# Kernel optimization log

Hardware: AMD Instinct MI355X
Metric: run time of the kernel (lower is better)

## Reference

```python
import jax, jax.numpy as jnp
import numpy as np

# ---- constants from module defaults ----
IMG, PS, STRIDE, C_IN = 224, 16, 8, 1
NP1D = (IMG - PS) // STRIDE + 1          # 27
NUM_PATCHES = NP1D * NP1D                # 729
EMBED = 64
N_INPUT = NUM_PATCHES * EMBED            # 46656
N_HIDDEN = 1000                          # d_model
N_RNN = 100
N_STEPS = 5
BETA, THR = 0.8, 0.5
BETA_R, THR_R = 0.95, 1.0
LM_SPN = 0.0058
ALPHA = 2.0  # snntorch ATan surrogate default

@jax.custom_vjp
def spike(x):
    return (x > 0).astype(x.dtype)

def _spike_fwd(x):
    return spike(x), x

def _spike_bwd(x, g):
    # snntorch ATan surrogate gradient
    return (g * (ALPHA / 2.0) / (1.0 + (jnp.pi / 2.0 * ALPHA * x) ** 2),)

spike.defvjp(_spike_fwd, _spike_bwd)

def extract_patches(x):
    # x: [B, C, H, W] -> [B, num_patches, C*PS*PS] matching torch unfold+permute+flatten
    B, C, H, W = x.shape
    idx = (jnp.arange(NP1D)[:, None] * STRIDE + jnp.arange(PS)).reshape(-1)  # [NP1D*PS]
    t = x[:, :, idx, :].reshape(B, C, NP1D, PS, W)
    t = t[..., idx].reshape(B, C, NP1D, PS, NP1D, PS)
    t = t.transpose(0, 2, 4, 1, 3, 5)  # [B, nh, nw, C, ph, pw]
    return t.reshape(B, NUM_PATCHES, C * PS * PS)

def setup_inputs() -> dict:
    key = jax.random.key(0)
    ks = jax.random.split(key, 12)
    def lin(k, fi, fo):
        kw, kb = jax.random.split(k)
        s = 1.0 / np.sqrt(fi)
        return (jax.random.uniform(kw, (fi, fo), jnp.float32, -s, s),
                jax.random.uniform(kb, (fo,), jnp.float32, -s, s))
    W_pe, b_pe = lin(ks[0], C_IN * PS * PS, EMBED)
    pos_embed = 0.02 * jax.random.normal(ks[1], (1, NUM_PATCHES, EMBED), jnp.float32)
    W1, b1 = lin(ks[2], N_INPUT, N_HIDDEN)
    W2, b2 = lin(ks[3], N_HIDDEN, N_HIDDEN)
    W3, b3 = lin(ks[4], N_HIDDEN, N_HIDDEN)
    WR, bR = lin(ks[5], N_HIDDEN, N_RNN)
    Vw, Vb = lin(ks[6], N_RNN, N_RNN)      # RLeaky recurrent linear
    Wq, bq = lin(ks[7], N_RNN, N_HIDDEN)
    Wk, bk = lin(ks[8], N_HIDDEN, N_HIDDEN)
    Wv, bv = lin(ks[9], N_HIDDEN, N_HIDDEN)
    Wo, bo = lin(ks[10], N_HIDDEN, 1)       # cross_last=True -> output_proj to 1
    data = jax.random.normal(ks[11], (32, C_IN, IMG, IMG), jnp.float32)
    return {"data": data, "W_pe": W_pe, "b_pe": b_pe, "pos_embed": pos_embed,
            "W1": W1, "b1": b1, "W2": W2, "b2": b2, "W3": W3, "b3": b3,
            "WR": WR, "bR": bR, "Vw": Vw, "Vb": Vb,
            "Wq": Wq, "bq": bq, "Wk": Wk, "bk": bk, "Wv": Wv, "bv": bv,
            "Wo": Wo, "bo": bo}

def _forward(data, W_pe, b_pe, pos_embed, W1, b1, W2, b2, W3, b3,
             WR, bR, Vw, Vb, Wq, bq, Wk, bk, Wv, bv, Wo, bo):
    B = data.shape[0]
    patches = extract_patches(data)                      # [B, 729, 256]
    x = patches @ W_pe + b_pe + pos_embed               # [B, 729, 64]
    x_flat = x.reshape(B, -1)                            # [B, 46656]
    cur1 = x_flat @ W1 + b1                              # constant across steps
    scale = jnp.sqrt(jnp.asarray(N_HIDDEN, jnp.float32))  # head_dim = d_model (1 head)

    def leaky(mem, cur, beta=BETA, thr=THR):
        reset = jax.lax.stop_gradient(spike(mem - thr))
        mem = beta * mem + cur - reset * thr
        return mem, spike(mem - thr)

    def step(carry, t):
        mem1, mem2, mem3, spk_r, mem_r, mem_out, total, prev, reg = carry
        # layers[:2] call -- first Leaky1 update
        mem1, spk1 = leaky(mem1, cur1)
        # layers[:7] call -- Leaky1 state updated a SECOND time (same x_flat)
        mem1, spk1b = leaky(mem1, cur1)
        mem2, spk2 = leaky(mem2, spk1b @ W2 + b2)
        mem3, spk3 = leaky(mem3, spk2 @ W3 + b3)  # Dropout is identity in eval
        total = total + spk1.mean() + spk3.mean()
        # RLeaky (beta=0.95, threshold=1.0, subtract reset, recurrent linear)
        rlin = spk1 @ WR + bR
        reset_r = jax.lax.stop_gradient(spike(mem_r - THR_R))
        mem_r = BETA_R * mem_r + rlin + spk_r @ Vw + Vb - reset_r * THR_R
        spk_r = spike(mem_r - THR_R)
        total = total + spk_r.mean()
        # cross-attention: feature dim acts as the sequence dim (seq=1 in view)
        q = spk_r @ Wq + bq                               # [B, 1000]
        k = spk3 @ Wk + bk                                # [B, 1000]
        v = spk3 @ Wv + bv                                # [B, 1000]
        probs = jax.nn.softmax(q[:, :, None] * k[:, None, :] / scale, axis=-1)  # [B,1000,1000]
        att = jnp.einsum('bij,bj->bi', probs, v) @ Wo + bo  # [B, 1]
        mem_out, spk_out = leaky(mem_out, att)
        mem_out = jax.lax.stop_gradient(mem_out)          # .detach() in source
        total = total + spk_out.mean()
        reg = reg + LM_SPN * total + jnp.where(t > 0, LM_SPN * jnp.abs(total - prev), 0.0)
        return (mem1, mem2, mem3, spk_r, mem_r, mem_out, total, total, reg), spk_out

    z = jnp.float32(0.0)
    init = (jnp.zeros((B, N_HIDDEN)), jnp.zeros((B, N_HIDDEN)), jnp.zeros((B, N_HIDDEN)),
            jnp.zeros((B, N_RNN)), jnp.zeros((B, N_RNN)), jnp.zeros((B, 1)), z, z, z)
    carry, spk_rec = jax.lax.scan(step, init, jnp.arange(N_STEPS))
    out = spk_rec.sum(0)[:, 0] / N_STEPS                  # [B]
    reg_norm = carry[-1] / N_STEPS
    return out, reg_norm

def reference(data, W_pe, b_pe, pos_embed, W1, b1, W2, b2, W3, b3,
              WR, bR, Vw, Vb, Wq, bq, Wk, bk, Wv, bv, Wo, bo):
    return _forward(data, W_pe, b_pe, pos_embed, W1, b1, W2, b2, W3, b3,
                    WR, bR, Vw, Vb, Wq, bq, Wk, bk, Wv, bv, Wo, bo)
```

## Files before the change

kernel.cpp:

```cpp
#include <hip/hip_runtime.h>

#define OFF_X     0
#define OFF_CUR1  1492992
#define OFF_MEM1  1524992
#define OFF_MEM2  1556992
#define OFF_MEM3  1588992
#define OFF_SPK1B 1652992
#define OFF_MEMR  1844992
#define OFF_SPKR  1848192
#define OFF_MEMO  1851392
#define OFF_PATT  1851424
#define OFF_CNT   1851680
#define OFF_OACC  1851700
#define OFF_SC    1851732
#define OFF_TICK  1851736
#define OFF_PART  1851744
#define OFF_PG2   OFF_PART
#define OFF_PG3   (OFF_PART + 800000)
#define OFF_PKK   (OFF_PART + 1600000)
#define OFF_PVV   (OFF_PART + 2400000)
#define OFF_M2B   (OFF_PART + 3200000)
#define OFF_M3B   (OFF_PART + 3232000)

static constexpr float kBETA  = 0.8f;
static constexpr float kTHR   = 0.5f;
static constexpr float kBETAR = 0.95f;
static constexpr float kTHRR  = 1.0f;
static constexpr float kLM    = 0.0058f;

__global__ void k_init(float* ws) {
    int idx = blockIdx.x * 256 + threadIdx.x;
    if (idx < 96000) {
        ws[OFF_MEM1 + idx] = 0.f;
    } else {
        int j = idx - 96000;
        if (j < 6752) ws[OFF_MEMR + j] = 0.f;
    }
}

__global__ __launch_bounds__(64) void k_patch(
    const float* __restrict__ data, const float* __restrict__ Wpe,
    const float* __restrict__ bpe, const float* __restrict__ pos,
    float* __restrict__ xf)
{
    int b = blockIdx.x, pr = blockIdx.y;
    int tid = threadIdx.x;
    const float* db = data + (size_t)b * 50176 + pr * 1792;
    float bb = bpe[tid];
    float acc[27];
    #pragma unroll
    for (int pc = 0; pc < 27; ++pc)
        acc[pc] = bb + pos[(pr * 27 + pc) * 64 + tid];
    #pragma unroll 2
    for (int c = 0; c < 256; ++c) {
        float w = Wpe[c * 64 + tid];
        const float* row = db + (c >> 4) * 224 + (c & 15);
        #pragma unroll
        for (int pc = 0; pc < 27; ++pc)
            acc[pc] = fmaf(row[pc * 8], w, acc[pc]);
    }
    size_t obase = (size_t)b * 46656 + (size_t)pr * 27 * 64 + tid;
    #pragma unroll
    for (int pc = 0; pc < 27; ++pc)
        xf[obase + (size_t)pc * 64] = acc[pc];
}

__global__ __launch_bounds__(256) void k_gemm1_part(
    const float* __restrict__ xf, const float* __restrict__ W1,
    float* __restrict__ part, int tpc)
{
    int chunk = blockIdx.x;
    int hg = blockIdx.y;
    int t0 = chunk * tpc;
    int t1 = t0 + tpc; if (t1 > 729) t1 = 729;
    int tid = threadIdx.x;
    __shared__ float xs[2048];
    float acc[32][2];
    #pragma unroll
    for (int b = 0; b < 32; ++b) { acc[b][0] = 0.f; acc[b][1] = 0.f; }

    const int hbase = hg * 500;
    const bool ok1 = (tid + 256) < 500;
    const int h0 = hbase + tid;
    const int h1 = hbase + (ok1 ? tid + 256 : 0);
    for (int tt = t0; tt < t1; ++tt) {
        int i0 = tt * 64;
        __syncthreads();
        for (int l = tid; l < 2048; l += 256)
            xs[l] = xf[(size_t)(l >> 6) * 46656 + i0 + (l & 63)];
        __syncthreads();
        for (int ii4 = 0; ii4 < 16; ++ii4) {
            int i = i0 + ii4 * 4;
            const float* c0 = W1 + (size_t)i * 1000 + h0;
            const float* c1 = W1 + (size_t)i * 1000 + h1;
            float w0a = c0[0], w1a = c0[1000], w2a = c0[2000], w3a = c0[3000];
            float w0b = ok1 ? c1[0]    : 0.f;
            float w1b = ok1 ? c1[1000] : 0.f;
            float w2b = ok1 ? c1[2000] : 0.f;
            float w3b = ok1 ? c1[3000] : 0.f;
            #pragma unroll
            for (int b = 0; b < 32; ++b) {
                float4 xv = *reinterpret_cast<const float4*>(&xs[b * 64 + ii4 * 4]);
                float a0 = acc[b][0], a1 = acc[b][1];
                a0 = fmaf(xv.x, w0a, a0);  a1 = fmaf(xv.x, w0b, a1);
                a0 = fmaf(xv.y, w1a, a0);  a1 = fmaf(xv.y, w1b, a1);
                a0 = fmaf(xv.z, w2a, a0);  a1 = fmaf(xv.z, w2b, a1);
                a0 = fmaf(xv.w, w3a, a0);  a1 = fmaf(xv.w, w3b, a1);
                acc[b][0] = a0; acc[b][1] = a1;
            }
        }
    }
    float* pc = part + (size_t)chunk * 32000 + hbase;
    #pragma unroll
    for (int b = 0; b < 32; ++b) {
        pc[b * 1000 + tid] = acc[b][0];
        if (ok1) pc[b * 1000 + tid + 256] = acc[b][1];
    }
}

__global__ void k_gemm1_reduce(const float* __restrict__ part,
                               const float* __restrict__ b1,
                               float* __restrict__ cur1, int nchunk)
{
    int idx = blockIdx.x * 128 + threadIdx.x;
    if (idx >= 32000) return;
    int h = idx % 1000;
    float a0 = b1[h], a1 = 0.f, a2 = 0.f, a3 = 0.f;
    int c = 0;
    for (; c + 4 <= nchunk; c += 4) {
        a0 += part[(size_t)c * 32000 + idx];
        a1 += part[(size_t)(c + 1) * 32000 + idx];
        a2 += part[(size_t)(c + 2) * 32000 + idx];
        a3 += part[(size_t)(c + 3) * 32000 + idx];
    }
    for (; c < nchunk; ++c) a0 += part[(size_t)c * 32000 + idx];
    cur1[idx] = (a0 + a1) + (a2 + a3);
}

__global__ __launch_bounds__(512) void k_stepR(
    const float* __restrict__ cur1, float* __restrict__ mem1,
    float* __restrict__ spk1b,
    const float* __restrict__ WR, const float* __restrict__ bR,
    const float* __restrict__ Vw, const float* __restrict__ Vb,
    float* __restrict__ mem_r, float* __restrict__ spk_r,
    float* cnt0, float* cnt2)
{
    int b = blockIdx.x;
    int tid = threadIdx.x;
    __shared__ float s1[1000];
    __shared__ float sr[100];
    __shared__ float red2[4][128];
    __shared__ float csum[8];

    float localc = 0.f;
    if (tid < 250) {
        int base = b * 1000 + tid * 4;
        float4 m4 = *reinterpret_cast<const float4*>(&mem1[base]);
        float4 c4 = *reinterpret_cast<const float4*>(&cur1[base]);
        float mm[4] = {m4.x, m4.y, m4.z, m4.w};
        float cc[4] = {c4.x, c4.y, c4.z, c4.w};
        float mb[4], sb[4];
        #pragma unroll
        for (int q = 0; q < 4; ++q) {
            float m = mm[q], c = cc[q];
            float r1 = (m - kTHR > 0.f) ? kTHR : 0.f;
            float ma = __fsub_rn(__fadd_rn(__fmul_rn(kBETA, m), c), r1);
            float s  = (ma - kTHR > 0.f) ? 1.f : 0.f;
            float r2 = __fmul_rn(s, kTHR);
            float mv = __fsub_rn(__fadd_rn(__fmul_rn(kBETA, ma), c), r2);
            sb[q] = (mv - kTHR > 0.f) ? 1.f : 0.f;
            mb[q] = mv;
            s1[tid * 4 + q] = s;
            localc += s;
        }
        *reinterpret_cast<float4*>(&mem1[base])  = make_float4(mb[0], mb[1], mb[2], mb[3]);
        *reinterpret_cast<float4*>(&spk1b[base]) = make_float4(sb[0], sb[1], sb[2], sb[3]);
    }
    if (tid < 100) sr[tid] = spk_r[b * 100 + tid];
    for (int off = 32; off; off >>= 1) localc += __shfl_down(localc, off, 64);
    if ((tid & 63) == 0) csum[tid >> 6] = localc;
    __syncthreads();
    if (tid == 0) {
        float cs = 0.f;
        #pragma unroll
        for (int w = 0; w < 8; ++w) cs += csum[w];
        atomicAdd(cnt0, cs);
    }

    int ks = tid >> 7, hh = tid & 127;
    float p = 0.f;
    if (hh < 100) {
        const float* wp = WR + (size_t)(ks * 250) * 100 + hh;
        int j0 = ks * 250;
        #pragma unroll 5
        for (int j = 0; j < 250; ++j) p = fmaf(s1[j0 + j], wp[(size_t)j * 100], p);
    }
    red2[ks][hh] = p;
    __syncthreads();
    float s = 0.f;
    if (tid < 100) {
        float acc = bR[tid] + ((red2[0][tid] + red2[1][tid]) + (red2[2][tid] + red2[3][tid]));
        float rec = 0.f;
        for (int j = 0; j < 100; ++j) rec = fmaf(sr[j], Vw[j * 100 + tid], rec);
        float m = mem_r[b * 100 + tid];
        float r = (m - kTHRR > 0.f) ? kTHRR : 0.f;
        float mn = __fsub_rn(__fadd_rn(__fadd_rn(__fadd_rn(__fmul_rn(kBETAR, m), acc), rec), Vb[tid]), r);
        s = (mn - kTHRR > 0.f) ? 1.f : 0.f;
        mem_r[b * 100 + tid] = mn;
        spk_r[b * 100 + tid] = s;
    }
    unsigned long long msk = __ballot(s > 0.5f);
    if ((tid & 63) == 0) {
        int pc2 = __popcll(msk);
        if (pc2) atomicAdd(cnt2, (float)pc2);
    }
}

__global__ __launch_bounds__(256) void k_gsp(
    const float* __restrict__ A, const float* __restrict__ W,
    float* __restrict__ part)
{
    int hb = blockIdx.x, kc = blockIdx.y, bg = blockIdx.z;
    int tid = threadIdx.x;
    int j0 = kc * 40;
    __shared__ __align__(16) float al[320];
    __shared__ float redg[8 * 128];
    for (int l = tid; l < 320; l += 256)
        al[l] = A[(size_t)(bg * 8 + (l & 7)) * 1000 + j0 + (l >> 3)];
    __syncthreads();
    int ks = tid >> 7, hh = tid & 127;
    float acc[8];
    #pragma unroll
    for (int b = 0; b < 8; ++b) acc[b] = 0.f;
    if (hh < 125) {
        int h = hb * 125 + hh;
        const float* Wp = W + (size_t)(j0 + ks * 20) * 1000 + h;
        const float4* abase = reinterpret_cast<const float4*>(&al[ks * 20 * 8]);
        #pragma unroll 4
        for (int jj = 0; jj < 20; ++jj) {
            float w = Wp[(size_t)jj * 1000];
            const float4* a4 = abase + jj * 2;
            #pragma unroll
            for (int q = 0; q < 2; ++q) {
                float4 av = a4[q];
                acc[q * 4 + 0] = fmaf(av.x, w, acc[q * 4 + 0]);
                acc[q * 4 + 1] = fmaf(av.y, w, acc[q * 4 + 1]);
                acc[q * 4 + 2] = fmaf(av.z, w, acc[q * 4 + 2]);
                acc[q * 4 + 3] = fmaf(av.w, w, acc[q * 4 + 3]);
            }
        }
    }
    if (ks == 1 && hh < 125) {
        #pragma unroll
        for (int b = 0; b < 8; ++b) redg[b * 128 + hh] = acc[b];
    }
    __syncthreads();
    if (ks == 0 && hh < 125) {
        int h = hb * 125 + hh;
        float* pp = part + (size_t)kc * 32000 + (size_t)(bg * 8) * 1000 + h;
        #pragma unroll
        for (int b = 0; b < 8; ++b) pp[(size_t)b * 1000] = acc[b] + redg[b * 128 + hh];
    }
}

template <bool COUNT>
__global__ __launch_bounds__(256) void k_gspred(
    const float* __restrict__ pin, const float* __restrict__ bias,
    const float* __restrict__ mem_old, float* __restrict__ mem_new,
    const float* __restrict__ W, float* __restrict__ pout, float* cnt)
{
    int hs = blockIdx.x, kc = blockIdx.y, bg = blockIdx.z;
    int tid = threadIdx.x;
    int j0 = kc * 40;
    __shared__ __align__(16) float al[320];
    __shared__ float redg[8 * 128];
    __shared__ float csum[4];
    float localc = 0.f;
    for (int e = tid; e < 320; e += 256) {
        int jj = e % 40, bi = e / 40;
        int idx = (bg * 8 + bi) * 1000 + j0 + jj;
        float a = bias[j0 + jj];
        #pragma unroll 5
        for (int c = 0; c < 25; ++c) a += pin[(size_t)c * 32000 + idx];
        float m = mem_old[idx];
        float r = (m - kTHR > 0.f) ? kTHR : 0.f;
        float mn = __fsub_rn(__fadd_rn(__fmul_rn(kBETA, m), a), r);
        float s = (mn - kTHR > 0.f) ? 1.f : 0.f;
        al[jj * 8 + bi] = s;
        if (hs == 0) { mem_new[idx] = mn; localc += s; }
    }
    if (COUNT) {
        for (int off = 32; off; off >>= 1) localc += __shfl_down(localc, off, 64);
        if ((tid & 63) == 0) csum[tid >> 6] = localc;
    }
    __syncthreads();
    if (COUNT && tid == 0 && hs == 0) {
        float tot = csum[0] + csum[1] + csum[2] + csum[3];
        if (tot != 0.f) atomicAdd(cnt, tot);
    }
    int ks = tid >> 7, hh = tid & 127;
    float acc[8];
    #pragma unroll
    for (int b = 0; b < 8; ++b) acc[b] = 0.f;
    if (hh < 125) {
        int h = hs * 125 + hh;
        const float* Wp = W + (size_t)(j0 + ks * 20) * 1000 + h;
        const float4* abase = reinterpret_cast<const float4*>(&al[ks * 20 * 8]);
        #pragma unroll 4
        for (int jj = 0; jj < 20; ++jj) {
            float w = Wp[(size_t)jj * 1000];
            const float4* a4 = abase + jj * 2;
            #pragma unroll
            for (int q = 0; q < 2; ++q) {
                float4 av = a4[q];
                acc[q * 4 + 0] = fmaf(av.x, w, acc[q * 4 + 0]);
                acc[q * 4 + 1] = fmaf(av.y, w, acc[q * 4 + 1]);
                acc[q * 4 + 2] = fmaf(av.z, w, acc[q * 4 + 2]);
                acc[q * 4 + 3] = fmaf(av.w, w, acc[q * 4 + 3]);
            }
        }
    }
    if (ks == 1 && hh < 125) {
        #pragma unroll
        for (int b = 0; b < 8; ++b) redg[b * 128 + hh] = acc[b];
    }
    __syncthreads();
    if (ks == 0 && hh < 125) {
        int h = hs * 125 + hh;
        float* pp = pout + (size_t)kc * 32000 + (size_t)(bg * 8) * 1000 + h;
        #pragma unroll
        for (int b = 0; b < 8; ++b) pp[(size_t)b * 1000] = acc[b] + redg[b * 128 + hh];
    }
}

__global__ __launch_bounds__(256) void k_gspred_kv(
    const float* __restrict__ pin, const float* __restrict__ bias,
    const float* __restrict__ mem_old, float* __restrict__ mem_new,
    const float* __restrict__ Wk, const float* __restrict__ Wv,
    float* __restrict__ pk, float* __restrict__ pv, float* cnt)
{
    int hs = blockIdx.x, kc = blockIdx.y, bg = blockIdx.z;
    int tid = threadIdx.x;
    int j0 = kc * 40;
    __shared__ __align__(16) float al[320];
    __shared__ float redk[8 * 128];
    __shared__ float redv[8 * 128];
    __shared__ float csum[4];
    float localc = 0.f;
    for (int e = tid; e < 320; e += 256) {
        int jj = e % 40, bi = e / 40;
        int idx = (bg * 8 + bi) * 1000 + j0 + jj;
        float a = bias[j0 + jj];
        #pragma unroll 5
        for (int c = 0; c < 25; ++c) a += pin[(size_t)c * 32000 + idx];
        float m = mem_old[idx];
        float r = (m - kTHR > 0.f) ? kTHR : 0.f;
        float mn = __fsub_rn(__fadd_rn(__fmul_rn(kBETA, m), a), r);
        float s = (mn - kTHR > 0.f) ? 1.f : 0.f;
        al[jj * 8 + bi] = s;
        if (hs == 0) { mem_new[idx] = mn; localc += s; }
    }
    for (int off = 32; off; off >>= 1) localc += __shfl_down(localc, off, 64);
    if ((tid & 63) == 0) csum[tid >> 6] = localc;
    __syncthreads();
    if (tid == 0 && hs == 0) {
        float tot = csum[0] + csum[1] + csum[2] + csum[3];
        if (tot != 0.f) atomicAdd(cnt, tot);
    }
    int ks = tid >> 7, hh = tid & 127;
    float ak[8], av2[8];
    #pragma unroll
    for (int b = 0; b < 8; ++b) { ak[b] = 0.f; av2[b] = 0.f; }
    if (hh < 125) {
        int h = hs * 125 + hh;
        const float* wkp = Wk + (size_t)(j0 + ks * 20) * 1000 + h;
        const float* wvp = Wv + (size_t)(j0 + ks * 20) * 1000 + h;
        const float4* abase = reinterpret_cast<const float4*>(&al[ks * 20 * 8]);
        #pragma unroll 4
        for (int jj = 0; jj < 20; ++jj) {
            float wk = wkp[(size_t)jj * 1000];
            float wv = wvp[(size_t)jj * 1000];
            const float4* a4 = abase + jj * 2;
            #pragma unroll
            for (int q = 0; q < 2; ++q) {
                float4 av = a4[q];
                ak[q * 4 + 0] = fmaf(av.x, wk, ak[q * 4 + 0]);
                ak[q * 4 + 1] = fmaf(av.y, wk, ak[q * 4 + 1]);
                ak[q * 4 + 2] = fmaf(av.z, wk, ak[q * 4 + 2]);
                ak[q * 4 + 3] = fmaf(av.w, wk, ak[q * 4 + 3]);
                av2[q * 4 + 0] = fmaf(av.x, wv, av2[q * 4 + 0]);
                av2[q * 4 + 1] = fmaf(av.y, wv, av2[q * 4 + 1]);
                av2[q * 4 + 2] = fmaf(av.z, wv, av2[q * 4 + 2]);
                av2[q * 4 + 3] = fmaf(av.w, wv, av2[q * 4 + 3]);
            }
        }
    }
    if (ks == 1 && hh < 125) {
        #pragma unroll
        for (int b = 0; b < 8; ++b) { redk[b * 128 + hh] = ak[b]; redv[b * 128 + hh] = av2[b]; }
    }
    __syncthreads();
    if (ks == 0 && hh < 125) {
        int h = hs * 125 + hh;
        float* ppk = pk + (size_t)kc * 32000 + (size_t)(bg * 8) * 1000 + h;
        float* ppv = pv + (size_t)kc * 32000 + (size_t)(bg * 8) * 1000 + h;
        #pragma unroll
        for (int b = 0; b < 8; ++b) {
            ppk[(size_t)b * 1000] = ak[b] + redk[b * 128 + hh];
            ppv[(size_t)b * 1000] = av2[b] + redv[b * 128 + hh];
        }
    }
}

__global__ __launch_bounds__(512) void k_attnred(
    const float* __restrict__ pkk, const float* __restrict__ pvv,
    const float* __restrict__ bk, const float* __restrict__ bv,
    const float* __restrict__ spkr, const float* __restrict__ Wq,
    const float* __restrict__ bq, const float* __restrict__ Wo,
    const float* __restrict__ bo,
    float* __restrict__ patt, float* __restrict__ memo,
    float* __restrict__ oacc, const float* __restrict__ cnt,
    float* __restrict__ sc, float* __restrict__ dout,
    unsigned int* __restrict__ tick, int t)
{
    int it = blockIdx.x, b = blockIdx.y;
    int tid = threadIdx.x;
    __shared__ float kk[1000], vv[1000];
    __shared__ float sr[100];
    __shared__ float red[512];
    __shared__ float pden[512], pnum[512];
    __shared__ int isLast;
    float pmax = -3.4e38f, pmin = 3.4e38f;
    if (tid < 100) sr[tid] = spkr[b * 100 + tid];
    for (int h = tid; h < 1000; h += 512) {
        int idx = b * 1000 + h;
        float ak = bk[h], av = bv[h];
        #pragma unroll 5
        for (int c = 0; c < 25; ++c) {
            ak += pkk[(size_t)c * 32000 + idx];
            av += pvv[(size_t)c * 32000 + idx];
        }
        kk[h] = ak; vv[h] = av;
        pmax = fmaxf(pmax, ak);
        pmin = fminf(pmin, ak);
    }
    red[tid] = pmax;
    __syncthreads();
    for (int s2 = 256; s2 > 0; s2 >>= 1) {
        if (tid < s2) red[tid] = fmaxf(red[tid], red[tid + s2]);
        __syncthreads();
    }
    float kmax = red[0];
    __syncthreads();
    red[tid] = pmin;
    __syncthreads();
    for (int s2 = 256; s2 > 0; s2 >>= 1) {
        if (tid < s2) red[tid] = fminf(red[tid], red[tid + s2]);
        __syncthreads();
    }
    float kmin = red[0];
    __syncthreads();

    int quarter = tid >> 7, lane = tid & 127;
    float den = 0.f, num = 0.f;
    if (lane < 125) {
        int i = it * 125 + lane;
        float qi = bq[i];
        for (int j = 0; j < 100; ++j) qi = fmaf(sr[j], Wq[j * 1000 + i], qi);
        float qs = qi / 31.62277660168379f;
        float m = (qs >= 0.f) ? qs * kmax : qs * kmin;
        int jb = quarter * 250;
        for (int j = 0; j < 250; ++j) {
            float e = __expf(fmaf(qs, kk[jb + j], -m));
            den += e;
            num = fmaf(e, vv[jb + j], num);
        }
    }
    pden[tid] = den; pnum[tid] = num;
    __syncthreads();
    float pw = 0.f;
    if (tid < 125) {
        float dsum = (pden[tid] + pden[tid + 128]) + (pden[tid + 256] + pden[tid + 384]);
        float nsum = (pnum[tid] + pnum[tid + 128]) + (pnum[tid + 256] + pnum[tid + 384]);
        pw = (nsum / dsum) * Wo[it * 125 + tid];
    }
    red[tid] = (tid < 125) ? pw : 0.f;
    __syncthreads();
    for (int s2 = 256; s2 > 0; s2 >>= 1) {
        if (tid < s2) red[tid] += red[tid + s2];
        __syncthreads();
    }
    if (tid == 0) patt[b * 8 + it] = red[0];
    __syncthreads();
    if (tid == 0) {
        __threadfence();
        unsigned r = atomicAdd(tick, 1u);
        isLast = (r == 255u) ? 1 : 0;
    }
    __syncthreads();
    if (isLast && tid < 64) {
        __threadfence();
        float s = 0.f;
        if (tid < 32) {
            float a = bo[0];
            for (int itx = 0; itx < 8; ++itx) a += patt[tid * 8 + itx];
            float m = memo[tid];
            float r = (m - kTHR > 0.f) ? kTHR : 0.f;
            float mn = __fsub_rn(__fadd_rn(__fmul_rn(kBETA, m), a), r);
            memo[tid] = mn;
            s = (mn - kTHR > 0.f) ? 1.f : 0.f;
            float oa = oacc[tid] + s;
            oacc[tid] = oa;
            if (t == 4) dout[tid] = oa / 5.0f;
        }
        unsigned long long msk = __ballot(s > 0.5f);
        float co = (float)__popcll(msk);
        if (tid == 0) {
            float total = sc[0];
            float prev = total;
            total = __fadd_rn(total, __fdiv_rn(cnt[0], 32000.f));
            total = __fadd_rn(total, __fdiv_rn(cnt[1], 32000.f));
            total = __fadd_rn(total, __fdiv_rn(cnt[2], 3200.f));
            total = __fadd_rn(total, __fdiv_rn(co, 32.f));
            float reg = sc[1];
            reg = __fadd_rn(reg, __fmul_rn(kLM, total));
            if (t > 0) reg = __fadd_rn(reg, __fmul_rn(kLM, fabsf(__fsub_rn(total, prev))));
            sc[0] = total; sc[1] = reg;
            if (t == 4) dout[32] = reg / 5.0f;
        }
    }
}

extern "C" void kernel_launch(void* const* d_in, const int* in_sizes, int n_in,
                              void* d_out, int out_size, void* d_ws, size_t ws_size,
                              hipStream_t stream)
{
    const float* data = (const float*)d_in[0];
    const float* Wpe  = (const float*)d_in[1];
    const float* bpe  = (const float*)d_in[2];
    const float* pos  = (const float*)d_in[3];
    const float* W1   = (const float*)d_in[4];
    const float* b1   = (const float*)d_in[5];
    const float* W2   = (const float*)d_in[6];
    const float* b2   = (const float*)d_in[7];
    const float* W3   = (const float*)d_in[8];
    const float* b3   = (const float*)d_in[9];
    const float* WR   = (const float*)d_in[10];
    const float* bR   = (const float*)d_in[11];
    const float* Vw   = (const float*)d_in[12];
    const float* Vb   = (const float*)d_in[13];
    const float* Wq   = (const float*)d_in[14];
    const float* bq   = (const float*)d_in[15];
    const float* Wk   = (const float*)d_in[16];
    const float* bk   = (const float*)d_in[17];
    const float* Wv   = (const float*)d_in[18];
    const float* bv   = (const float*)d_in[19];
    const float* Wo   = (const float*)d_in[20];
    const float* bo   = (const float*)d_in[21];

    float* ws = (float*)d_ws;
    float* dout = (float*)d_out;

    float* xf    = ws + OFF_X;
    float* cur1  = ws + OFF_CUR1;
    float* mem1  = ws + OFF_MEM1;
    float* mem2a = ws + OFF_MEM2;
    float* mem3a = ws + OFF_MEM3;
    float* spk1b = ws + OFF_SPK1B;
    float* memr  = ws + OFF_MEMR;
    float* spkr  = ws + OFF_SPKR;
    float* memo  = ws + OFF_MEMO;
    float* patt  = ws + OFF_PATT;
    float* cntb  = ws + OFF_CNT;
    float* oacc  = ws + OFF_OACC;
    float* sc    = ws + OFF_SC;
    unsigned int* tick = (unsigned int*)(ws + OFF_TICK);
    float* part  = ws + OFF_PART;
    float* pg2   = ws + OFF_PG2;
    float* pg3   = ws + OFF_PG3;
    float* pkk   = ws + OFF_PKK;
    float* pvv   = ws + OFF_PVV;
    float* mem2b = ws + OFF_M2B;
    float* mem3b = ws + OFF_M3B;

    size_t ws_f = ws_size / 4;
    size_t avail = (ws_f > OFF_PART) ? (ws_f - OFF_PART) : 0;
    long nchunk_l = (long)(avail / 32000);
    int nchunk = (nchunk_l > 365) ? 365 : (int)nchunk_l;
    if (nchunk < 1) nchunk = 1;
    int tpc = (729 + nchunk - 1) / nchunk;
    nchunk = (729 + tpc - 1) / tpc;

    k_init<<<402, 256, 0, stream>>>(ws);
    k_patch<<<dim3(32, 27), 64, 0, stream>>>(data, Wpe, bpe, pos, xf);
    k_gemm1_part<<<dim3(nchunk, 2), 256, 0, stream>>>(xf, W1, part, tpc);
    k_gemm1_reduce<<<250, 128, 0, stream>>>(part, b1, cur1, nchunk);

    for (int t = 0; t < 5; ++t) {
        float* cnt = cntb + t * 4;
        float* m2o = (t & 1) ? mem2b : mem2a;
        float* m2n = (t & 1) ? mem2a : mem2b;
        float* m3o = (t & 1) ? mem3b : mem3a;
        float* m3n = (t & 1) ? mem3a : mem3b;

        k_stepR<<<32, 512, 0, stream>>>(cur1, mem1, spk1b, WR, bR, Vw, Vb,
                                        memr, spkr, cnt + 0, cnt + 2);
        k_gsp<<<dim3(8, 25, 4), 256, 0, stream>>>(spk1b, W2, pg2);
        k_gspred<false><<<dim3(8, 25, 4), 256, 0, stream>>>(
            pg2, b2, m2o, m2n, W3, pg3, nullptr);
        k_gspred_kv<<<dim3(8, 25, 4), 256, 0, stream>>>(
            pg3, b3, m3o, m3n, Wk, Wv, pkk, pvv, cnt + 1);
        k_attnred<<<dim3(8, 32), 512, 0, stream>>>(
            pkk, pvv, bk, bv, spkr, Wq, bq, Wo, bo,
            patt, memo, oacc, cnt, sc, dout, tick + t, t);
    }
    (void)in_sizes; (void)n_in; (void)out_size;
}
```

Measured before the change: 525.8 us.

## Fuse layer-1 leaky update into W2 GEMM and recurrent step into attention kernel

Removes the separate k_stepR launch per timestep. The leaky neuron update for layer 1 is recomputed inside each k_gsp block for its own slice, with only hb==0 blocks writing state back. The recurrent RLeaky step is recomputed redundantly in every k_attnred block, with only it==0 blocks writing. mem1, mem_r and spk_r are now double-buffered so these redundant recomputations stay race-free. This saves five launches and their serialization, at the cost of duplicated WR/Vw matvec work across 8 attention blocks per batch.

New measurement: 517.7 us. Within noise of the previous version (-1.5%).

```diff
diff --git a/kernel.cpp b/kernel.cpp
--- a/kernel.cpp
+++ b/kernel.cpp
@@ -5,7 +5,6 @@
 #define OFF_MEM1  1524992
 #define OFF_MEM2  1556992
 #define OFF_MEM3  1588992
-#define OFF_SPK1B 1652992
 #define OFF_MEMR  1844992
 #define OFF_SPKR  1848192
 #define OFF_MEMO  1851392
@@ -21,6 +20,10 @@
 #define OFF_PVV   (OFF_PART + 2400000)
 #define OFF_M2B   (OFF_PART + 3200000)
 #define OFF_M3B   (OFF_PART + 3232000)
+#define OFF_M1B   (OFF_PART + 3264000)
+#define OFF_SPK1  (OFF_PART + 3296000)
+#define OFF_MRB   (OFF_PART + 3328000)
+#define OFF_SRB   (OFF_PART + 3331200)
 
 static constexpr float kBETA  = 0.8f;
 static constexpr float kTHR   = 0.5f;
@@ -137,97 +140,38 @@
     cur1[idx] = (a0 + a1) + (a2 + a3);
 }
 
-__global__ __launch_bounds__(512) void k_stepR(
-    const float* __restrict__ cur1, float* __restrict__ mem1,
-    float* __restrict__ spk1b,
-    const float* __restrict__ WR, const float* __restrict__ bR,
-    const float* __restrict__ Vw, const float* __restrict__ Vb,
-    float* __restrict__ mem_r, float* __restrict__ spk_r,
-    float* cnt0, float* cnt2)
-{
-    int b = blockIdx.x;
-    int tid = threadIdx.x;
-    __shared__ float s1[1000];
-    __shared__ float sr[100];
-    __shared__ float red2[4][128];
-    __shared__ float csum[8];
-
-    float localc = 0.f;
-    if (tid < 250) {
-        int base = b * 1000 + tid * 4;
-        float4 m4 = *reinterpret_cast<const float4*>(&mem1[base]);
-        float4 c4 = *reinterpret_cast<const float4*>(&cur1[base]);
-        float mm[4] = {m4.x, m4.y, m4.z, m4.w};
-        float cc[4] = {c4.x, c4.y, c4.z, c4.w};
-        float mb[4], sb[4];
-        #pragma unroll
-        for (int q = 0; q < 4; ++q) {
-            float m = mm[q], c = cc[q];
-            float r1 = (m - kTHR > 0.f) ? kTHR : 0.f;
-            float ma = __fsub_rn(__fadd_rn(__fmul_rn(kBETA, m), c), r1);
-            float s  = (ma - kTHR > 0.f) ? 1.f : 0.f;
-            float r2 = __fmul_rn(s, kTHR);
-            float mv = __fsub_rn(__fadd_rn(__fmul_rn(kBETA, ma), c), r2);
-            sb[q] = (mv - kTHR > 0.f) ? 1.f : 0.f;
-            mb[q] = mv;
-            s1[tid * 4 + q] = s;
-            localc += s;
-        }
-        *reinterpret_cast<float4*>(&mem1[base])  = make_float4(mb[0], mb[1], mb[2], mb[3]);
-        *reinterpret_cast<float4*>(&spk1b[base]) = make_float4(sb[0], sb[1], sb[2], sb[3]);
-    }
-    if (tid < 100) sr[tid] = spk_r[b * 100 + tid];
-    for (int off = 32; off; off >>= 1) localc += __shfl_down(localc, off, 64);
-    if ((tid & 63) == 0) csum[tid >> 6] = localc;
-    __syncthreads();
-    if (tid == 0) {
-        float cs = 0.f;
-        #pragma unroll
-        for (int w = 0; w < 8; ++w) cs += csum[w];
-        atomicAdd(cnt0, cs);
-    }
-
-    int ks = tid >> 7, hh = tid & 127;
-    float p = 0.f;
-    if (hh < 100) {
-        const float* wp = WR + (size_t)(ks * 250) * 100 + hh;
-        int j0 = ks * 250;
-        #pragma unroll 5
-        for (int j = 0; j < 250; ++j) p = fmaf(s1[j0 + j], wp[(size_t)j * 100], p);
-    }
-    red2[ks][hh] = p;
-    __syncthreads();
-    float s = 0.f;
-    if (tid < 100) {
-        float acc = bR[tid] + ((red2[0][tid] + red2[1][tid]) + (red2[2][tid] + red2[3][tid]));
-        float rec = 0.f;
-        for (int j = 0; j < 100; ++j) rec = fmaf(sr[j], Vw[j * 100 + tid], rec);
-        float m = mem_r[b * 100 + tid];
-        float r = (m - kTHRR > 0.f) ? kTHRR : 0.f;
-        float mn = __fsub_rn(__fadd_rn(__fadd_rn(__fadd_rn(__fmul_rn(kBETAR, m), acc), rec), Vb[tid]), r);
-        s = (mn - kTHRR > 0.f) ? 1.f : 0.f;
-        mem_r[b * 100 + tid] = mn;
-        spk_r[b * 100 + tid] = s;
-    }
-    unsigned long long msk = __ballot(s > 0.5f);
-    if ((tid & 63) == 0) {
-        int pc2 = __popcll(msk);
-        if (pc2) atomicAdd(cnt2, (float)pc2);
-    }
-}
-
 __global__ __launch_bounds__(256) void k_gsp(
-    const float* __restrict__ A, const float* __restrict__ W,
-    float* __restrict__ part)
+    const float* __restrict__ cur1, const float* __restrict__ mem1_old,
+    float* __restrict__ mem1_new, float* __restrict__ spk1_out,
+    const float* __restrict__ W, float* __restrict__ part, float* cnt0)
 {
     int hb = blockIdx.x, kc = blockIdx.y, bg = blockIdx.z;
     int tid = threadIdx.x;
     int j0 = kc * 40;
     __shared__ __align__(16) float al[320];
     __shared__ float redg[8 * 128];
-    for (int l = tid; l < 320; l += 256)
-        al[l] = A[(size_t)(bg * 8 + (l & 7)) * 1000 + j0 + (l >> 3)];
-    __syncthreads();
+    __shared__ float csum[4];
+    float localc = 0.f;
+    for (int e = tid; e < 320; e += 256) {
+        int jj = e % 40, bi = e / 40;
+        int idx = (bg * 8 + bi) * 1000 + j0 + jj;
+        float m = mem1_old[idx], c = cur1[idx];
+        float r1 = (m - kTHR > 0.f) ? kTHR : 0.f;
+        float ma = __fsub_rn(__fadd_rn(__fmul_rn(kBETA, m), c), r1);
+        float s1 = (ma - kTHR > 0.f) ? 1.f : 0.f;
+        float r2 = __fmul_rn(s1, kTHR);
+        float mb = __fsub_rn(__fadd_rn(__fmul_rn(kBETA, ma), c), r2);
+        float s1b = (mb - kTHR > 0.f) ? 1.f : 0.f;
+        al[jj * 8 + bi] = s1b;
+        if (hb == 0) { mem1_new[idx] = mb; spk1_out[idx] = s1; localc += s1; }
+    }
+    for (int off = 32; off; off >>= 1) localc += __shfl_down(localc, off, 64);
+    if ((tid & 63) == 0) csum[tid >> 6] = localc;
+    __syncthreads();
+    if (hb == 0 && tid == 0) {
+        float tot = csum[0] + csum[1] + csum[2] + csum[3];
+        if (tot != 0.f) atomicAdd(cnt0, tot);
+    }
     int ks = tid >> 7, hh = tid & 127;
     float acc[8];
     #pragma unroll
@@ -415,23 +359,64 @@
 __global__ __launch_bounds__(512) void k_attnred(
     const float* __restrict__ pkk, const float* __restrict__ pvv,
     const float* __restrict__ bk, const float* __restrict__ bv,
-    const float* __restrict__ spkr, const float* __restrict__ Wq,
-    const float* __restrict__ bq, const float* __restrict__ Wo,
-    const float* __restrict__ bo,
+    const float* __restrict__ spk1, const float* __restrict__ WR,
+    const float* __restrict__ bR, const float* __restrict__ Vw,
+    const float* __restrict__ Vb,
+    const float* __restrict__ memr_old, float* __restrict__ memr_new,
+    const float* __restrict__ spkr_old, float* __restrict__ spkr_new,
+    const float* __restrict__ Wq, const float* __restrict__ bq,
+    const float* __restrict__ Wo, const float* __restrict__ bo,
     float* __restrict__ patt, float* __restrict__ memo,
     float* __restrict__ oacc, const float* __restrict__ cnt,
     float* __restrict__ sc, float* __restrict__ dout,
-    unsigned int* __restrict__ tick, int t)
+    unsigned int* __restrict__ tick, float* cnt2, int t)
 {
     int it = blockIdx.x, b = blockIdx.y;
     int tid = threadIdx.x;
     __shared__ float kk[1000], vv[1000];
     __shared__ float sr[100];
+    __shared__ float s1l[1000];
+    __shared__ float red2[512];
     __shared__ float red[512];
     __shared__ float pden[512], pnum[512];
     __shared__ int isLast;
+
+    for (int l = tid; l < 1000; l += 512) s1l[l] = spk1[b * 1000 + l];
+    if (tid < 100) sr[tid] = spkr_old[b * 100 + tid];
+    __syncthreads();
+    int ks4 = tid >> 7, hh4 = tid & 127;
+    float p = 0.f;
+    if (hh4 < 100) {
+        const float* wp = WR + (size_t)(ks4 * 250) * 100 + hh4;
+        int j0r = ks4 * 250;
+        #pragma unroll 5
+        for (int j = 0; j < 250; ++j) p = fmaf(s1l[j0r + j], wp[(size_t)j * 100], p);
+    }
+    red2[ks4 * 128 + hh4] = p;
+    __syncthreads();
+    float snew = 0.f;
+    if (tid < 100) {
+        float acc = bR[tid] + ((red2[tid] + red2[128 + tid]) + (red2[256 + tid] + red2[384 + tid]));
+        float rec = 0.f;
+        for (int j = 0; j < 100; ++j) rec = fmaf(sr[j], Vw[j * 100 + tid], rec);
+        float m = memr_old[b * 100 + tid];
+        float r = (m - kTHRR > 0.f) ? kTHRR : 0.f;
+        float mn = __fsub_rn(__fadd_rn(__fadd_rn(__fadd_rn(__fmul_rn(kBETAR, m), acc), rec), Vb[tid]), r);
+        snew = (mn - kTHRR > 0.f) ? 1.f : 0.f;
+        if (it == 0) { memr_new[b * 100 + tid] = mn; spkr_new[b * 100 + tid] = snew; }
+    }
+    if (it == 0) {
+        unsigned long long mskr = __ballot(snew > 0.5f);
+        if ((tid & 63) == 0) {
+            int pc2 = __popcll(mskr);
+            if (pc2) atomicAdd(cnt2, (float)pc2);
+        }
+    }
+    __syncthreads();
+    if (tid < 100) sr[tid] = snew;
+    __syncthreads();
+
     float pmax = -3.4e38f, pmin = 3.4e38f;
-    if (tid < 100) sr[tid] = spkr[b * 100 + tid];
     for (int h = tid; h < 1000; h += 512) {
         int idx = b * 1000 + h;
         float ak = bk[h], av = bv[h];
@@ -563,12 +548,11 @@
 
     float* xf    = ws + OFF_X;
     float* cur1  = ws + OFF_CUR1;
-    float* mem1  = ws + OFF_MEM1;
+    float* mem1a = ws + OFF_MEM1;
     float* mem2a = ws + OFF_MEM2;
     float* mem3a = ws + OFF_MEM3;
-    float* spk1b = ws + OFF_SPK1B;
-    float* memr  = ws + OFF_MEMR;
-    float* spkr  = ws + OFF_SPKR;
+    float* memra = ws + OFF_MEMR;
+    float* spkra = ws + OFF_SPKR;
     float* memo  = ws + OFF_MEMO;
     float* patt  = ws + OFF_PATT;
     float* cntb  = ws + OFF_CNT;
@@ -582,6 +566,10 @@
     float* pvv   = ws + OFF_PVV;
     float* mem2b = ws + OFF_M2B;
     float* mem3b = ws + OFF_M3B;
+    float* mem1b = ws + OFF_M1B;
+    float* spk1  = ws + OFF_SPK1;
+    float* memrb = ws + OFF_MRB;
+    float* spkrb = ws + OFF_SRB;
 
     size_t ws_f = ws_size / 4;
     size_t avail = (ws_f > OFF_PART) ? (ws_f - OFF_PART) : 0;
@@ -598,21 +586,27 @@
 
     for (int t = 0; t < 5; ++t) {
         float* cnt = cntb + t * 4;
+        float* m1o = (t & 1) ? mem1b : mem1a;
+        float* m1n = (t & 1) ? mem1a : mem1b;
         float* m2o = (t & 1) ? mem2b : mem2a;
         float* m2n = (t & 1) ? mem2a : mem2b;
         float* m3o = (t & 1) ? mem3b : mem3a;
         float* m3n = (t & 1) ? mem3a : mem3b;
-
-        k_stepR<<<32, 512, 0, stream>>>(cur1, mem1, spk1b, WR, bR, Vw, Vb,
-                                        memr, spkr, cnt + 0, cnt + 2);
-        k_gsp<<<dim3(8, 25, 4), 256, 0, stream>>>(spk1b, W2, pg2);
+        float* mro = (t & 1) ? memrb : memra;
+        float* mrn = (t & 1) ? memra : memrb;
+        float* sro = (t & 1) ? spkrb : spkra;
+        float* srn = (t & 1) ? spkra : spkrb;
+
+        k_gsp<<<dim3(8, 25, 4), 256, 0, stream>>>(
+            cur1, m1o, m1n, spk1, W2, pg2, cnt + 0);
         k_gspred<false><<<dim3(8, 25, 4), 256, 0, stream>>>(
             pg2, b2, m2o, m2n, W3, pg3, nullptr);
         k_gspred_kv<<<dim3(8, 25, 4), 256, 0, stream>>>(
             pg3, b3, m3o, m3n, Wk, Wv, pkk, pvv, cnt + 1);
         k_attnred<<<dim3(8, 32), 512, 0, stream>>>(
-            pkk, pvv, bk, bv, spkr, Wq, bq, Wo, bo,
-            patt, memo, oacc, cnt, sc, dout, tick + t, t);
+            pkk, pvv, bk, bv, spk1, WR, bR, Vw, Vb,
+            mro, mrn, sro, srn, Wq, bq, Wo, bo,
+            patt, memo, oacc, cnt, sc, dout, tick + t, cnt + 2, t);
     }
     (void)in_sizes; (void)n_in; (void)out_size;
 }
```
